# Kernel optimization log

Measured on AMD Instinct MI355X. Metric: run time of the kernel, lower is better.

Reference implementation:

```python
import jax, jax.numpy as jnp
import numpy as np

H = 16
EMB = 1024
DH = 64  # att_dim


def setup_inputs() -> dict:
    key = jax.random.key(0)
    k1, k2, k3 = jax.random.split(key, 3)
    B, T = 4, 2048
    x = jax.random.normal(k1, (B, T, EMB), dtype=jnp.float32)
    # torch nn.Linear weight layout: [out_features, in_features]
    w_qkv = jax.random.normal(k2, (3 * H * DH, EMB), dtype=jnp.float32) * (1.0 / np.sqrt(EMB))
    wo = jax.random.normal(k3, (EMB, H * DH), dtype=jnp.float32) * (1.0 / np.sqrt(H * DH))
    return {"x": x, "w_qkv": w_qkv, "wo": wo}


def reference(x, w_qkv, wo):
    B, T, C = x.shape
    qkv = jnp.einsum('btc,oc->bto', x, w_qkv)  # [B,T,3*H*DH]
    q, k, v = jnp.split(qkv, 3, axis=-1)
    # [B,H,T,DH]
    q = q.reshape(B, T, H, DH).transpose(0, 2, 1, 3)
    k = k.reshape(B, T, H, DH).transpose(0, 2, 1, 3)
    v = v.reshape(B, T, H, DH).transpose(0, 2, 1, 3)
    scale = 1.0 / np.sqrt(DH).astype(np.float32)
    scores = jnp.einsum('bhqd,bhkd->bhqk', q, k) * scale
    causal = jnp.tril(jnp.ones((T, T), dtype=bool))
    scores = jnp.where(causal, scores, jnp.finfo(scores.dtype).min)
    attn = jax.nn.softmax(scores, axis=-1)
    y = jnp.einsum('bhqk,bhkd->bhqd', attn, v)  # [B,H,T,DH]
    y = y.transpose(0, 2, 1, 3).reshape(B, T, H * DH)
    return jnp.einsum('bti,oi->bto', y, wo)
```

## Files before the change

kernel.cpp:

```cpp
#include <hip/hip_runtime.h>
#include <hip/hip_bf16.h>
#include <stdint.h>


typedef __attribute__((ext_vector_type(8))) short short8;
typedef __attribute__((ext_vector_type(4))) float floatx4;

extern "C" __device__ float __ocml_native_exp2_f32(float);

__device__ __forceinline__ ushort f2bf(float f) {
  uint32_t u = __float_as_uint(f);
  u += 0x7fff + ((u >> 16) & 1);
  return (ushort)(u >> 16);
}

#if __has_builtin(__builtin_amdgcn_cvt_pk_bf16_f32)
typedef __attribute__((ext_vector_type(2))) __bf16 bf16x2;
__device__ __forceinline__ uint32_t pack_bf16(float a, float b) {
  union { bf16x2 v; uint32_t u; } cv;
  cv.v = __builtin_amdgcn_cvt_pk_bf16_f32(a, b);
  return cv.u;
}
#else
__device__ __forceinline__ uint32_t pack_bf16(float a, float b) {
  uint32_t ua = __float_as_uint(a) + 0x8000u;
  uint32_t ub = __float_as_uint(b) + 0x8000u;
  return __builtin_amdgcn_perm(ub, ua, 0x07060302u);
}
#endif

__device__ __forceinline__ void gload16(const ushort* g, ushort* l) {
  __builtin_amdgcn_global_load_lds(
      (const __attribute__((address_space(1))) void*)g,
      (__attribute__((address_space(3))) void*)l, 16, 0, 0);
}

__global__ __launch_bounds__(256) void cvt3_kernel(const float* __restrict__ x,
                                                   const float* __restrict__ wq,
                                                   const float* __restrict__ wo,
                                                   ushort* __restrict__ xo,
                                                   ushort* __restrict__ wqo,
                                                   ushort* __restrict__ woo) {
  int i = blockIdx.x * 256 + threadIdx.x;
  const float* in; ushort* out; int idx;
  if (i < 2097152)      { in = x;  out = xo;  idx = i; }
  else if (i < 2883584) { in = wq; out = wqo; idx = i - 2097152; }
  else                  { in = wo; out = woo; idx = i - 2883584; }
  float4 v = ((const float4*)in)[idx];
  ushort4 o;
  o.x = f2bf(v.x); o.y = f2bf(v.y); o.z = f2bf(v.z); o.w = f2bf(v.w);
  ((ushort4*)out)[idx] = o;
}

template<int MODE>
__global__ __launch_bounds__(256) void gemm_bt(const ushort* __restrict__ A,
                                               const ushort* __restrict__ Bw,
                                               float* __restrict__ Cf,
                                               ushort* __restrict__ qb,
                                               ushort* __restrict__ kb,
                                               ushort* __restrict__ vt) {
  constexpr int CS = 136;
  constexpr int SMEM_N = (MODE == 0) ? 128 * CS : 128 * 64 * 2;
  __shared__ ushort smem[SMEM_N];
  ushort* As = smem;
  ushort* Bs = smem + 128 * 64;
  int tid = threadIdx.x;
  int lane = tid & 63, wave = tid >> 6;
  int lrow = lane & 15, quad = lane >> 4;
  int wr = (wave >> 1) * 64, wc = (wave & 1) * 64;
  int m0 = blockIdx.x * 128, n0 = blockIdx.y * 128;

  const floatx4 zero4 = {0.f, 0.f, 0.f, 0.f};
  floatx4 acc[4][4];
#pragma unroll
  for (int i = 0; i < 4; i++)
#pragma unroll
    for (int j = 0; j < 4; j++) acc[i][j] = zero4;

  int rsub = tid >> 3;
  int colb = (((tid & 7) ^ (rsub & 7)) * 8);
  const ushort* Ag = A + (size_t)(m0 + rsub) * 1024 + colb;
  const ushort* Bg = Bw + (size_t)(n0 + rsub) * 1024 + colb;
  int fo = (quad ^ (lrow & 7)) * 8;

  for (int kk = 0; kk < 1024; kk += 64) {
    __syncthreads();
#pragma unroll
    for (int i = 0; i < 4; i++) {
      gload16(Ag + kk + (size_t)i * 32 * 1024, &As[(8 * wave + 32 * i) * 64]);
      gload16(Bg + kk + (size_t)i * 32 * 1024, &Bs[(8 * wave + 32 * i) * 64]);
    }
    __syncthreads();
#pragma unroll
    for (int ks = 0; ks < 2; ks++) {
      short8 a[4], b[4];
#pragma unroll
      for (int i = 0; i < 4; i++)
        a[i] = *(const short8*)(&As[(wr + i * 16 + lrow) * 64 + (fo ^ (32 * ks))]);
#pragma unroll
      for (int j = 0; j < 4; j++)
        b[j] = *(const short8*)(&Bs[(wc + j * 16 + lrow) * 64 + (fo ^ (32 * ks))]);
#pragma unroll
      for (int i = 0; i < 4; i++)
#pragma unroll
        for (int j = 0; j < 4; j++)
          acc[i][j] = __builtin_amdgcn_mfma_f32_16x16x32_bf16(a[i], b[j], acc[i][j], 0, 0, 0);
    }
  }

  if (MODE == 1) {
#pragma unroll
    for (int i = 0; i < 4; i++)
#pragma unroll
      for (int j = 0; j < 4; j++)
#pragma unroll
        for (int r = 0; r < 4; r++) {
          int m = m0 + wr + i * 16 + quad * 4 + r;
          int n = n0 + wc + j * 16 + lrow;
          Cf[(size_t)m * 1024 + n] = acc[i][j][r];
        }
    return;
  }

  int sec = n0 >> 10;
  __syncthreads();

  if (sec < 2) {
    float qs = (sec == 0) ? 0.18033688f : 1.0f;
#pragma unroll
    for (int i = 0; i < 4; i++)
#pragma unroll
      for (int j = 0; j < 4; j++)
#pragma unroll
        for (int r = 0; r < 4; r++)
          smem[(wr + i * 16 + quad * 4 + r) * CS + wc + j * 16 + lrow] =
              f2bf(acc[i][j][r] * qs);
    __syncthreads();
    ushort* dst = (sec == 0) ? qb : kb;
    int mrow = tid >> 3, kcol = tid & 7;
#pragma unroll
    for (int mi = 0; mi < 4; mi++)
#pragma unroll
      for (int hh = 0; hh < 2; hh++) {
        int mloc = mi * 32 + mrow;
        uint4 val = *(const uint4*)(&smem[mloc * CS + hh * 64 + kcol * 8]);
        int m = m0 + mloc, b = m >> 11, t = m & 2047;
        int h = ((n0 + hh * 64) & 1023) >> 6;
        *(uint4*)(dst + ((size_t)(b * 16 + h) * 2048 + t) * 64 + kcol * 8) = val;
      }
  } else {
#pragma unroll
    for (int i = 0; i < 4; i++)
#pragma unroll
      for (int j = 0; j < 4; j++) {
        uint2 w;
        w.x = pack_bf16(acc[i][j][0], acc[i][j][1]);
        w.y = pack_bf16(acc[i][j][2], acc[i][j][3]);
        *(uint2*)(&smem[(wc + j * 16 + lrow) * CS + wr + i * 16 + quad * 4]) = w;
      }
    __syncthreads();
    int b = m0 >> 11, t0 = m0 & 2047;
    int drow = tid >> 4, kcol = tid & 15;
#pragma unroll
    for (int di = 0; di < 8; di++) {
      int nloc = di * 16 + drow;
      uint4 val = *(const uint4*)(&smem[nloc * CS + kcol * 8]);
      int n = n0 + nloc;
      int h = (n & 1023) >> 6, d = n & 63;
      *(uint4*)(vt + ((size_t)(b * 16 + h) * 64 + d) * 2048 + t0 + kcol * 8) = val;
    }
  }
}

__global__ __launch_bounds__(512) void attn_kernel(const ushort* __restrict__ qg,
                                                   const ushort* __restrict__ kg,
                                                   const ushort* __restrict__ vg,
                                                   ushort* __restrict__ y) {
  __shared__ ushort Ks[64 * 64];
  __shared__ ushort Vs[64 * 64];
  __shared__ ushort Ps[8 * 16 * 72];
  int tid = threadIdx.x;
  int lane = tid & 63, wave = tid >> 6;
  int lrow = lane & 15, quad = lane >> 4;
  int gx = blockIdx.x, gy = blockIdx.y;
  int pr = gy >> 3;
  int bh = (gy & 7) * 8 + gx;
  const ushort* qp = qg + (size_t)bh * 2048 * 64;
  const ushort* kp = kg + (size_t)bh * 2048 * 64;
  const ushort* vp = vg + (size_t)bh * 64 * 2048;
  int b = bh >> 4, h = bh & 15;
  int srow = tid >> 3, sc = tid & 7;
  int sswz = ((sc ^ (srow & 7)) * 8);
  int fo = (quad ^ (lrow & 7)) * 8;
  ushort* Pw = &Ps[wave * 16 * 72];

  const floatx4 zero4 = {0.f, 0.f, 0.f, 0.f};
  short8 ones;
#pragma unroll
  for (int i = 0; i < 8; i++) ones[i] = (short)0x3F80;

#pragma unroll 1
  for (int pass = 0; pass < 2; ++pass) {
    int qt = pass ? (15 - pr) : pr;
    int last = 2 * qt + 1;

    const ushort* qrow_p = qp + (size_t)((qt << 7) + wave * 16 + lrow) * 64;
    short8 a_q0 = *(const short8*)(qrow_p + quad * 8);
    short8 a_q1 = *(const short8*)(qrow_p + (quad ^ 4) * 8);

    uint4 kreg = *(const uint4*)(kp + (size_t)srow * 64 + sc * 8);
    uint4 vreg = *(const uint4*)(vp + (size_t)srow * 2048 + sc * 8);

    floatx4 l_acc = zero4;
    floatx4 o_acc[4];
#pragma unroll
    for (int j = 0; j < 4; j++) o_acc[j] = zero4;

#pragma unroll 1
    for (int kv = 0; kv <= last; kv++) {
      __syncthreads();
      *(uint4*)(&Ks[srow * 64 + sswz]) = kreg;
      *(uint4*)(&Vs[srow * 64 + sswz]) = vreg;
      if (kv < last) {
        kreg = *(const uint4*)(kp + (size_t)((kv + 1) * 64 + srow) * 64 + sc * 8);
        vreg = *(const uint4*)(vp + (size_t)srow * 2048 + (kv + 1) * 64 + sc * 8);
      }
      __syncthreads();

      floatx4 s[4];
#pragma unroll
      for (int ct = 0; ct < 4; ct++) {
        short8 k0 = *(const short8*)(&Ks[(ct * 16 + lrow) * 64 + fo]);
        short8 k1 = *(const short8*)(&Ks[(ct * 16 + lrow) * 64 + (fo ^ 32)]);
        floatx4 z = zero4;
        z = __builtin_amdgcn_mfma_f32_16x16x32_bf16(k0, a_q0, z, 0, 0, 0);
        z = __builtin_amdgcn_mfma_f32_16x16x32_bf16(k1, a_q1, z, 0, 0, 0);
        s[ct] = z;
      }

      if (kv >= 2 * qt) {
        int qabs = (qt << 7) + wave * 16 + lrow;
        int kbase = (kv << 6) + quad * 4;
#pragma unroll
        for (int ct = 0; ct < 4; ct++)
#pragma unroll
          for (int r = 0; r < 4; r++)
            if (kbase + ct * 16 + r > qabs) s[ct][r] = -1e30f;
      }

#pragma unroll
      for (int ct = 0; ct < 4; ct++) {
        float p0 = __ocml_native_exp2_f32(s[ct][0]);
        float p1 = __ocml_native_exp2_f32(s[ct][1]);
        float p2 = __ocml_native_exp2_f32(s[ct][2]);
        float p3 = __ocml_native_exp2_f32(s[ct][3]);
        uint2 w;
        w.x = pack_bf16(p0, p1);
        w.y = pack_bf16(p2, p3);
        *(uint2*)(&Pw[lrow * 72 + ct * 16 + quad * 4]) = w;
      }
      asm volatile("" ::: "memory");

      short8 a_p0 = *(const short8*)(&Pw[lrow * 72 + quad * 8]);
      short8 a_p1 = *(const short8*)(&Pw[lrow * 72 + 32 + quad * 8]);
      l_acc = __builtin_amdgcn_mfma_f32_16x16x32_bf16(a_p0, ones, l_acc, 0, 0, 0);
      l_acc = __builtin_amdgcn_mfma_f32_16x16x32_bf16(a_p1, ones, l_acc, 0, 0, 0);
#pragma unroll
      for (int j = 0; j < 4; j++) {
        short8 v0 = *(const short8*)(&Vs[(j * 16 + lrow) * 64 + fo]);
        short8 v1 = *(const short8*)(&Vs[(j * 16 + lrow) * 64 + (fo ^ 32)]);
        o_acc[j] = __builtin_amdgcn_mfma_f32_16x16x32_bf16(a_p0, v0, o_acc[j], 0, 0, 0);
        o_acc[j] = __builtin_amdgcn_mfma_f32_16x16x32_bf16(a_p1, v1, o_acc[j], 0, 0, 0);
      }
    }

    float inv[4];
#pragma unroll
    for (int r = 0; r < 4; r++) inv[r] = 1.0f / l_acc[r];

#pragma unroll
    for (int j = 0; j < 4; j++)
#pragma unroll
      for (int r = 0; r < 4; r++) {
        int t = (qt << 7) + wave * 16 + quad * 4 + r;
        y[((size_t)b * 2048 + t) * 1024 + h * 64 + j * 16 + lrow] =
            f2bf(o_acc[j][r] * inv[r]);
      }
  }
}

extern "C" void kernel_launch(void* const* d_in, const int* in_sizes, int n_in,
                              void* d_out, int out_size, void* d_ws, size_t ws_size,
                              hipStream_t stream) {
  const float* x     = (const float*)d_in[0];
  const float* w_qkv = (const float*)d_in[1];
  const float* wo    = (const float*)d_in[2];
  float* out = (float*)d_out;

  ushort* x_bf    = (ushort*)d_ws;
  ushort* wqkv_bf = x_bf + (size_t)8192 * 1024;
  ushort* wo_bf   = wqkv_bf + (size_t)3072 * 1024;
  ushort* qb      = wo_bf + (size_t)1024 * 1024;
  ushort* kb      = qb + (size_t)8388608;
  ushort* vt      = kb + (size_t)8388608;
  ushort* yb      = x_bf;

  cvt3_kernel<<<12288, 256, 0, stream>>>(x, w_qkv, wo, x_bf, wqkv_bf, wo_bf);
  gemm_bt<0><<<dim3(64, 24), 256, 0, stream>>>(x_bf, wqkv_bf, nullptr, qb, kb, vt);
  attn_kernel<<<dim3(8, 64), 512, 0, stream>>>(qb, kb, vt, yb);
  gemm_bt<1><<<dim3(64, 8), 256, 0, stream>>>(yb, wo_bf, out, nullptr, nullptr, nullptr);
}
```

Before: 219.5 us.

## Rewrite GEMMs as 256x128 tiles with 4-slot async LDS ring pipeline

Replaces the 128x128 single-buffered GEMM with a 512-thread, 256x128-tile kernel. It uses a four-slot LDS ring of 32-wide K tiles that keeps three tiles of global-to-LDS loads in flight, waits on them with explicit vmcnt, and raises wave priority around the MFMA block. The goal is to hide global load latency and get more reuse per tile. The epilogue is split into two halves that reuse the ring buffer for staging. In exchange, the grid has half as many blocks, the kernel uses more LDS per block, and the pipeline depends on hand-tuned waitcnt counts.

```diff
diff --git a/kernel.cpp b/kernel.cpp
--- a/kernel.cpp
+++ b/kernel.cpp
@@ -53,22 +53,27 @@
 }
 
 template<int MODE>
-__global__ __launch_bounds__(256) void gemm_bt(const ushort* __restrict__ A,
+__global__ __launch_bounds__(512) void gemm256(const ushort* __restrict__ A,
                                                const ushort* __restrict__ Bw,
                                                float* __restrict__ Cf,
                                                ushort* __restrict__ qb,
                                                ushort* __restrict__ kb,
                                                ushort* __restrict__ vt) {
-  constexpr int CS = 136;
-  constexpr int SMEM_N = (MODE == 0) ? 128 * CS : 128 * 64 * 2;
-  __shared__ ushort smem[SMEM_N];
-  ushort* As = smem;
-  ushort* Bs = smem + 128 * 64;
+  constexpr int SLOT = 12288;
+  __shared__ ushort ring[4 * SLOT];
   int tid = threadIdx.x;
   int lane = tid & 63, wave = tid >> 6;
   int lrow = lane & 15, quad = lane >> 4;
-  int wr = (wave >> 1) * 64, wc = (wave & 1) * 64;
-  int m0 = blockIdx.x * 128, n0 = blockIdx.y * 128;
+  int wm = wave >> 1, wn = wave & 1;
+  int wm64 = wm * 64, wn64 = wn * 64;
+  int m0 = blockIdx.x * 256, n0 = blockIdx.y * 128;
+
+  int srow = tid >> 2;
+  int schunk8 = ((tid & 3) ^ ((tid >> 3) & 3)) * 8;
+  const ushort* Ag0 = A + (size_t)(m0 + srow) * 1024 + schunk8;
+  const ushort* Ag1 = Ag0 + (size_t)128 * 1024;
+  const ushort* Bg0 = Bw + (size_t)(n0 + srow) * 1024 + schunk8;
+  int fo2 = (quad ^ ((lrow >> 1) & 3)) * 8;
 
   const floatx4 zero4 = {0.f, 0.f, 0.f, 0.f};
   floatx4 acc[4][4];
@@ -77,97 +82,120 @@
 #pragma unroll
     for (int j = 0; j < 4; j++) acc[i][j] = zero4;
 
-  int rsub = tid >> 3;
-  int colb = (((tid & 7) ^ (rsub & 7)) * 8);
-  const ushort* Ag = A + (size_t)(m0 + rsub) * 1024 + colb;
-  const ushort* Bg = Bw + (size_t)(n0 + rsub) * 1024 + colb;
-  int fo = (quad ^ (lrow & 7)) * 8;
-
-  for (int kk = 0; kk < 1024; kk += 64) {
-    __syncthreads();
-#pragma unroll
-    for (int i = 0; i < 4; i++) {
-      gload16(Ag + kk + (size_t)i * 32 * 1024, &As[(8 * wave + 32 * i) * 64]);
-      gload16(Bg + kk + (size_t)i * 32 * 1024, &Bs[(8 * wave + 32 * i) * 64]);
-    }
-    __syncthreads();
-#pragma unroll
-    for (int ks = 0; ks < 2; ks++) {
-      short8 a[4], b[4];
-#pragma unroll
-      for (int i = 0; i < 4; i++)
-        a[i] = *(const short8*)(&As[(wr + i * 16 + lrow) * 64 + (fo ^ (32 * ks))]);
-#pragma unroll
-      for (int j = 0; j < 4; j++)
-        b[j] = *(const short8*)(&Bs[(wc + j * 16 + lrow) * 64 + (fo ^ (32 * ks))]);
-#pragma unroll
-      for (int i = 0; i < 4; i++)
-#pragma unroll
-        for (int j = 0; j < 4; j++)
-          acc[i][j] = __builtin_amdgcn_mfma_f32_16x16x32_bf16(a[i], b[j], acc[i][j], 0, 0, 0);
-    }
+  auto stage = [&](int t) {
+    ushort* Sa = &ring[(t & 3) * SLOT];
+    size_t kk = (size_t)t * 32;
+    gload16(Ag0 + kk, &Sa[wave * 16 * 32]);
+    gload16(Ag1 + kk, &Sa[(128 + wave * 16) * 32]);
+    gload16(Bg0 + kk, &Sa[8192 + wave * 16 * 32]);
+  };
+
+#define KTILE(u_, N_, ISSUE_)                                                 \
+  {                                                                           \
+    ushort* As_ = &ring[((u_) & 3) * SLOT];                                   \
+    ushort* Bs_ = As_ + 8192;                                                 \
+    asm volatile("s_waitcnt vmcnt(" #N_ ")" ::: "memory");                    \
+    __syncthreads();                                                          \
+    short8 a_[4], b_[4];                                                      \
+    _Pragma("unroll")                                                         \
+    for (int mi = 0; mi < 4; mi++)                                            \
+      a_[mi] = *(const short8*)(&As_[(wm64 + mi * 16 + lrow) * 32 + fo2]);    \
+    _Pragma("unroll")                                                         \
+    for (int nj = 0; nj < 4; nj++)                                            \
+      b_[nj] = *(const short8*)(&Bs_[(wn64 + nj * 16 + lrow) * 32 + fo2]);    \
+    if (ISSUE_) stage((u_) + 3);                                              \
+    __builtin_amdgcn_s_setprio(1);                                            \
+    _Pragma("unroll")                                                         \
+    for (int mi = 0; mi < 4; mi++)                                            \
+      _Pragma("unroll")                                                       \
+      for (int nj = 0; nj < 4; nj++)                                          \
+        acc[mi][nj] = __builtin_amdgcn_mfma_f32_16x16x32_bf16(                \
+            a_[mi], b_[nj], acc[mi][nj], 0, 0, 0);                            \
+    __builtin_amdgcn_s_setprio(0);                                            \
   }
 
+  stage(0); stage(1); stage(2);
+#pragma unroll 1
+  for (int u = 0; u < 29; ++u) KTILE(u, 6, true);
+  KTILE(29, 6, false);
+  KTILE(30, 3, false);
+  KTILE(31, 0, false);
+#undef KTILE
+
   if (MODE == 1) {
 #pragma unroll
-    for (int i = 0; i < 4; i++)
-#pragma unroll
-      for (int j = 0; j < 4; j++)
+    for (int mi = 0; mi < 4; mi++)
+#pragma unroll
+      for (int nj = 0; nj < 4; nj++)
 #pragma unroll
         for (int r = 0; r < 4; r++) {
-          int m = m0 + wr + i * 16 + quad * 4 + r;
-          int n = n0 + wc + j * 16 + lrow;
-          Cf[(size_t)m * 1024 + n] = acc[i][j][r];
+          int m = m0 + wm64 + mi * 16 + quad * 4 + r;
+          int n = n0 + wn64 + nj * 16 + lrow;
+          Cf[(size_t)m * 1024 + n] = acc[mi][nj][r];
         }
     return;
   }
 
+  constexpr int CS = 136;
+  ushort* sm = ring;
   int sec = n0 >> 10;
+  int hrow = tid >> 4, kcol = tid & 15;
   __syncthreads();
 
   if (sec < 2) {
     float qs = (sec == 0) ? 0.18033688f : 1.0f;
-#pragma unroll
-    for (int i = 0; i < 4; i++)
-#pragma unroll
-      for (int j = 0; j < 4; j++)
-#pragma unroll
-        for (int r = 0; r < 4; r++)
-          smem[(wr + i * 16 + quad * 4 + r) * CS + wc + j * 16 + lrow] =
-              f2bf(acc[i][j][r] * qs);
-    __syncthreads();
     ushort* dst = (sec == 0) ? qb : kb;
-    int mrow = tid >> 3, kcol = tid & 7;
-#pragma unroll
-    for (int mi = 0; mi < 4; mi++)
-#pragma unroll
-      for (int hh = 0; hh < 2; hh++) {
-        int mloc = mi * 32 + mrow;
-        uint4 val = *(const uint4*)(&smem[mloc * CS + hh * 64 + kcol * 8]);
-        int m = m0 + mloc, b = m >> 11, t = m & 2047;
-        int h = ((n0 + hh * 64) & 1023) >> 6;
-        *(uint4*)(dst + ((size_t)(b * 16 + h) * 2048 + t) * 64 + kcol * 8) = val;
-      }
+    int hbase = n0 & 1023;
+#pragma unroll 1
+    for (int hf = 0; hf < 2; ++hf) {
+      if ((wm >> 1) == hf) {
+#pragma unroll
+        for (int mi = 0; mi < 4; mi++)
+#pragma unroll
+          for (int nj = 0; nj < 4; nj++)
+#pragma unroll
+            for (int r = 0; r < 4; r++)
+              sm[((wm & 1) * 64 + mi * 16 + quad * 4 + r) * CS +
+                 wn64 + nj * 16 + lrow] = f2bf(acc[mi][nj][r] * qs);
+      }
+      __syncthreads();
+#pragma unroll
+      for (int mi = 0; mi < 4; mi++) {
+        int mloc = mi * 32 + hrow;
+        int m = m0 + hf * 128 + mloc, b_ = m >> 11, t = m & 2047;
+        int col = kcol * 8;
+        int h = (hbase + col) >> 6, d = col & 63;
+        uint4 val = *(const uint4*)(&sm[mloc * CS + col]);
+        *(uint4*)(dst + ((size_t)(b_ * 16 + h) * 2048 + t) * 64 + d) = val;
+      }
+      __syncthreads();
+    }
   } else {
-#pragma unroll
-    for (int i = 0; i < 4; i++)
-#pragma unroll
-      for (int j = 0; j < 4; j++) {
-        uint2 w;
-        w.x = pack_bf16(acc[i][j][0], acc[i][j][1]);
-        w.y = pack_bf16(acc[i][j][2], acc[i][j][3]);
-        *(uint2*)(&smem[(wc + j * 16 + lrow) * CS + wr + i * 16 + quad * 4]) = w;
-      }
-    __syncthreads();
-    int b = m0 >> 11, t0 = m0 & 2047;
-    int drow = tid >> 4, kcol = tid & 15;
-#pragma unroll
-    for (int di = 0; di < 8; di++) {
-      int nloc = di * 16 + drow;
-      uint4 val = *(const uint4*)(&smem[nloc * CS + kcol * 8]);
-      int n = n0 + nloc;
-      int h = (n & 1023) >> 6, d = n & 63;
-      *(uint4*)(vt + ((size_t)(b * 16 + h) * 64 + d) * 2048 + t0 + kcol * 8) = val;
+    int b_ = m0 >> 11, t0 = m0 & 2047;
+#pragma unroll 1
+    for (int hf = 0; hf < 2; ++hf) {
+      if ((wm >> 1) == hf) {
+#pragma unroll
+        for (int mi = 0; mi < 4; mi++)
+#pragma unroll
+          for (int nj = 0; nj < 4; nj++) {
+            uint2 w;
+            w.x = pack_bf16(acc[mi][nj][0], acc[mi][nj][1]);
+            w.y = pack_bf16(acc[mi][nj][2], acc[mi][nj][3]);
+            *(uint2*)(&sm[(wn64 + nj * 16 + lrow) * CS +
+                          (wm & 1) * 64 + mi * 16 + quad * 4]) = w;
+          }
+      }
+      __syncthreads();
+#pragma unroll
+      for (int di = 0; di < 4; di++) {
+        int nloc = di * 32 + hrow;
+        int n = n0 + nloc, h = (n & 1023) >> 6, d = n & 63;
+        uint4 val = *(const uint4*)(&sm[nloc * CS + kcol * 8]);
+        *(uint4*)(vt + ((size_t)(b_ * 16 + h) * 64 + d) * 2048 +
+                  t0 + hf * 128 + kcol * 8) = val;
+      }
+      __syncthreads();
     }
   }
 }
@@ -306,7 +334,7 @@
   ushort* yb      = x_bf;
 
   cvt3_kernel<<<12288, 256, 0, stream>>>(x, w_qkv, wo, x_bf, wqkv_bf, wo_bf);
-  gemm_bt<0><<<dim3(64, 24), 256, 0, stream>>>(x_bf, wqkv_bf, nullptr, qb, kb, vt);
+  gemm256<0><<<dim3(32, 24), 512, 0, stream>>>(x_bf, wqkv_bf, nullptr, qb, kb, vt);
   attn_kernel<<<dim3(8, 64), 512, 0, stream>>>(qb, kb, vt, yb);
-  gemm_bt<1><<<dim3(64, 8), 256, 0, stream>>>(yb, wo_bf, out, nullptr, nullptr, nullptr);
-}
+  gemm256<1><<<dim3(32, 8), 512, 0, stream>>>(yb, wo_bf, out, nullptr, nullptr, nullptr);
+}
```

New measurement: 233.7 us. +6.5%, slower.
